# Optimization experiments

Measured on AMD Instinct MI355X. Metric: run time of the kernel, lower is better.

Reference implementation:

```python
import jax, jax.numpy as jnp
import numpy as np

B, S, H, E, TOPK = 8, 512, 1024, 8, 2


def setup_inputs() -> dict:
    key = jax.random.key(0)
    ks = jax.random.split(key, 10)
    D = 2 * H
    inp = {
        "vector": jax.random.normal(ks[0], (B, S, D), dtype=jnp.float32),
        # gate weights (Linear(H, E)): stored as [H, E] for x @ W + b
        "Wg": jax.random.normal(ks[1], (H, E), dtype=jnp.float32) * 0.02,
        "bg": jnp.zeros((E,), dtype=jnp.float32),
        "Wf": jax.random.normal(ks[2], (H, E), dtype=jnp.float32) * 0.02,
        "bf": jnp.zeros((E,), dtype=jnp.float32),
        # expert MLP weights, stacked over experts: Linear(2H,2H) -> ReLU -> Linear(2H,2H)
        "W1": jax.random.normal(ks[3], (E, D, D), dtype=jnp.float32) * 0.02,
        "b1": jnp.zeros((E, D), dtype=jnp.float32),
        "W2": jax.random.normal(ks[4], (E, D, D), dtype=jnp.float32) * 0.02,
        "b2": jnp.zeros((E, D), dtype=jnp.float32),
        # combine weights (config['initializer_weight'])
        "weight": jnp.ones((2,), dtype=jnp.float32),
        "top_k": TOPK,
    }
    return inp


def reference(vector, Wg, bg, Wf, bf, W1, b1, W2, b2, weight, top_k):
    h = Wg.shape[0]
    n_exp = Wg.shape[1]
    # gate_g on first half, softmax, then top-k sparsify (scatter of topk values)
    rout_g = jax.nn.softmax(vector[:, :, :h] @ Wg + bg, axis=-1)           # [B,S,E]
    vals, idx = jax.lax.top_k(rout_g, top_k)                               # [B,S,k]
    route_g = jnp.sum(jax.nn.one_hot(idx, n_exp, dtype=vals.dtype) * vals[..., None], axis=-2)  # [B,S,E]
    # gate_f on second half: dense softmax routing
    rout_f = jax.nn.softmax(vector[:, :, h:2 * h] @ Wf + bf, axis=-1)      # [B,S,E]
    # dense expert computation for every token (dropout = identity at eval)
    hidden = jax.nn.relu(jnp.einsum('bsd,edh->bseh', vector, W1) + b1)     # [B,S,E,2H]
    expert_out = jnp.einsum('bseh,ehd->bsed', hidden, W2) + b2             # [B,S,E,2H]
    out0 = weight[0] * jnp.einsum('bsed,bse->bsd', expert_out[..., :h], route_g)
    out1 = weight[1] * jnp.einsum('bsed,bse->bsd', expert_out[..., h:2 * h], rout_f)
    return (out0, out1)
```

## Files before the change

kernel.cpp:

```cpp
#include <hip/hip_runtime.h>

#define TOKENS 4096
#define DDIM   2048
#define HDIM   1024
#define NEXP   8
#define GK     2048
#define GN     2048

typedef __bf16 bf16_t;
typedef __bf16 bf16x8 __attribute__((ext_vector_type(8)));
typedef __bf16 bf16x4 __attribute__((ext_vector_type(4)));
typedef float  f32x4  __attribute__((ext_vector_type(4)));

__device__ inline void gld_lds16(const bf16_t* g, bf16_t* l) {
  __builtin_amdgcn_global_load_lds(
      (const __attribute__((address_space(1))) void*)g,
      (__attribute__((address_space(3))) void*)l, 16, 0, 0);
}

#define VMC(n)  asm volatile("s_waitcnt vmcnt(" #n ")" ::: "memory")
#define BAR()   __builtin_amdgcn_s_barrier()

__global__ __launch_bounds__(256)
void k_routing(const float* __restrict__ vec,
               const float* __restrict__ Wg, const float* __restrict__ bg,
               const float* __restrict__ Wf, const float* __restrict__ bfv,
               const float* __restrict__ wgt,
               float* __restrict__ c0, float* __restrict__ c1)
{
  const int wave = threadIdx.x >> 6;
  const int lane = threadIdx.x & 63;
  const int m = blockIdx.x * 4 + wave;
  const float* v = vec + (size_t)m * DDIM;

  float ag[NEXP], af[NEXP];
#pragma unroll
  for (int e = 0; e < NEXP; ++e) { ag[e] = 0.f; af[e] = 0.f; }

  for (int i = lane; i < HDIM; i += 64) {
    const float xg = v[i];
    const float xf = v[HDIM + i];
    const float4 wg0 = *(const float4*)(Wg + i * NEXP);
    const float4 wg1 = *(const float4*)(Wg + i * NEXP + 4);
    const float4 wf0 = *(const float4*)(Wf + i * NEXP);
    const float4 wf1 = *(const float4*)(Wf + i * NEXP + 4);
    ag[0] += xg * wg0.x; ag[1] += xg * wg0.y; ag[2] += xg * wg0.z; ag[3] += xg * wg0.w;
    ag[4] += xg * wg1.x; ag[5] += xg * wg1.y; ag[6] += xg * wg1.z; ag[7] += xg * wg1.w;
    af[0] += xf * wf0.x; af[1] += xf * wf0.y; af[2] += xf * wf0.z; af[3] += xf * wf0.w;
    af[4] += xf * wf1.x; af[5] += xf * wf1.y; af[6] += xf * wf1.z; af[7] += xf * wf1.w;
  }
#pragma unroll
  for (int e = 0; e < NEXP; ++e) {
#pragma unroll
    for (int off = 32; off >= 1; off >>= 1) {
      ag[e] += __shfl_xor(ag[e], off, 64);
      af[e] += __shfl_xor(af[e], off, 64);
    }
  }
  if (lane == 0) {
    float g[NEXP], f[NEXP];
    float mg = -1e30f, mf = -1e30f;
#pragma unroll
    for (int e = 0; e < NEXP; ++e) {
      g[e] = ag[e] + bg[e]; mg = fmaxf(mg, g[e]);
      f[e] = af[e] + bfv[e]; mf = fmaxf(mf, f[e]);
    }
    float sg = 0.f, sf = 0.f;
#pragma unroll
    for (int e = 0; e < NEXP; ++e) {
      g[e] = expf(g[e] - mg); sg += g[e];
      f[e] = expf(f[e] - mf); sf += f[e];
    }
    const float rg = 1.f / sg, rf = 1.f / sf;
#pragma unroll
    for (int e = 0; e < NEXP; ++e) { g[e] *= rg; f[e] *= rf; }
    int i1 = 0;
#pragma unroll
    for (int e = 1; e < NEXP; ++e) if (g[e] > g[i1]) i1 = e;
    int i2 = (i1 == 0) ? 1 : 0;
#pragma unroll
    for (int e = 0; e < NEXP; ++e) if (e != i1 && g[e] > g[i2]) i2 = e;
    const float w0 = wgt[0], w1 = wgt[1];
#pragma unroll
    for (int e = 0; e < NEXP; ++e) {
      c0[e * TOKENS + m] = (e == i1 || e == i2) ? w0 * g[e] : 0.f;
      c1[e * TOKENS + m] = w1 * f[e];
    }
  }
}

__global__ __launch_bounds__(256)
void k_cvt(const float* __restrict__ in, bf16_t* __restrict__ out)
{
  const size_t i = ((size_t)blockIdx.x * 256 + threadIdx.x) * 8;
  const float4 a = *(const float4*)(in + i);
  const float4 b = *(const float4*)(in + i + 4);
  bf16x8 o;
  o[0] = (bf16_t)a.x; o[1] = (bf16_t)a.y; o[2] = (bf16_t)a.z; o[3] = (bf16_t)a.w;
  o[4] = (bf16_t)b.x; o[5] = (bf16_t)b.y; o[6] = (bf16_t)b.z; o[7] = (bf16_t)b.w;
  *(bf16x8*)(out + i) = o;
}

#define TP 68
__global__ __launch_bounds__(256)
void k_cvt_wt(const float* __restrict__ W, bf16_t* __restrict__ Wt)
{
  __shared__ __attribute__((aligned(16))) bf16_t tile[64 * TP];
  const size_t eoff = (size_t)blockIdx.z * DDIM * DDIM;
  const float* w = W + eoff;
  bf16_t* wt = Wt + eoff;
  const int k0 = blockIdx.x * 64;
  const int n0 = blockIdx.y * 64;
  const int t = threadIdx.x;
  const int c4 = (t & 15) * 4;
  const int rb = (t >> 4) * 4;
#pragma unroll
  for (int rr = 0; rr < 4; ++rr) {
    const int r = rb + rr;
    const float4 v = *(const float4*)(w + (size_t)(k0 + r) * DDIM + n0 + c4);
    tile[(c4 + 0) * TP + r] = (bf16_t)v.x;
    tile[(c4 + 1) * TP + r] = (bf16_t)v.y;
    tile[(c4 + 2) * TP + r] = (bf16_t)v.z;
    tile[(c4 + 3) * TP + r] = (bf16_t)v.w;
  }
  __syncthreads();
  const int nl = t >> 2;
  const int kq = (t & 3) * 16;
  bf16_t* dst = wt + (size_t)(n0 + nl) * DDIM + k0 + kq;
#pragma unroll
  for (int j2 = 0; j2 < 4; ++j2) {
    bf16x4 u = *(const bf16x4*)(&tile[nl * TP + kq + j2 * 4]);
    *(bf16x4*)(dst + j2 * 4) = u;
  }
}


#define FRG(base, R, KQ) \
  (*(const bf16x8*)((base) + ((((R) * 32 + (KQ)) ^ ((((R) >> 3) & 1) << 4)))))

#define MFMA_(d, x, y) (d) = __builtin_amdgcn_mfma_f32_16x16x32_bf16((x), (y), (d), 0, 0, 0)

__global__ __launch_bounds__(512, 2)
void k_gemm1_8p(const bf16_t* __restrict__ A, const bf16_t* __restrict__ W1t,
                const float* __restrict__ b1, bf16_t* __restrict__ Hd)
{
  __shared__ __attribute__((aligned(16))) bf16_t AsF[4 * 8192];
  __shared__ __attribute__((aligned(16))) bf16_t BsF[4 * 8192];
  const int e = blockIdx.z;
  const int t = threadIdx.x;
  const int wave = t >> 6, lane = t & 63;
  const int m0 = blockIdx.x * 256, n0 = blockIdx.y * 256;
  const int wm = (wave >> 2) * 128, wn = (wave & 3) * 64;
  const int fr = lane & 15, kq = (lane >> 4) * 8;

  const int sRw = wave * 16 + (lane >> 2);
  const int sC  = ((lane & 3) * 8) ^ (((lane >> 5) & 1) << 4);
  const bf16_t* aSrc = A + (size_t)(m0 + sRw) * GK + sC;
  const bf16_t* bSrc = W1t + (size_t)e * GN * GK + (size_t)(n0 + sRw) * GK + sC;
  bf16_t* aDst = AsF + wave * 512;
  bf16_t* bDst = BsF + wave * 512;

#define STA1(P, U) do { const bf16_t* _s = aSrc + (size_t)(P) * 32; \
    gld_lds16(_s, aDst + (U) * 8192); \
    gld_lds16(_s + (size_t)128 * GK, aDst + (U) * 8192 + 4096); } while (0)
#define STB1(P, U) do { const bf16_t* _s = bSrc + (size_t)(P) * 32; \
    gld_lds16(_s, bDst + (U) * 8192); \
    gld_lds16(_s + (size_t)128 * GK, bDst + (U) * 8192 + 4096); } while (0)

  f32x4 acc[8][4] = {};

#define PH1(U, SP, SU, DOST) do { \
    bf16x8 a_[8], b_[4]; \
    _Pragma("unroll") \
    for (int _j = 0; _j < 4; ++_j) b_[_j] = FRG(BsF + (U) * 8192, wn + _j * 16 + fr, kq); \
    _Pragma("unroll") \
    for (int _i = 0; _i < 8; ++_i) a_[_i] = FRG(AsF + (U) * 8192, wm + _i * 16 + fr, kq); \
    if (DOST) { STA1(SP, SU); STB1(SP, SU); } \
    __builtin_amdgcn_s_setprio(1); \
    _Pragma("unroll") \
    for (int _i = 0; _i < 8; ++_i) \
      _Pragma("unroll") \
      for (int _j = 0; _j < 4; ++_j) MFMA_(acc[_i][_j], a_[_i], b_[_j]); \
    __builtin_amdgcn_s_setprio(0); \
  } while (0)

  STA1(0, 0); STB1(0, 0);
  STA1(1, 1); STB1(1, 1);
  STA1(2, 2); STB1(2, 2);
  VMC(8); BAR();

#pragma unroll 1
  for (int pb = 0; pb < 60; pb += 4) {
    PH1(0, pb + 3, 3, 1); VMC(8); BAR();
    PH1(1, pb + 4, 0, 1); VMC(8); BAR();
    PH1(2, pb + 5, 1, 1); VMC(8); BAR();
    PH1(3, pb + 6, 2, 1); VMC(8); BAR();
  }
  PH1(0, 63, 3, 1); VMC(8); BAR();
  PH1(1, 0, 0, 0);  VMC(4); BAR();
  PH1(2, 0, 0, 0);  VMC(0); BAR();
  PH1(3, 0, 0, 0);

  const float* bias = b1 + (size_t)e * DDIM;
  bf16_t* Hb = Hd + (size_t)e * TOKENS * DDIM;
  const int ecol = lane & 15, erow = (lane >> 4) * 4;
#pragma unroll
  for (int j = 0; j < 4; ++j) {
    const int gn = n0 + wn + j * 16 + ecol;
    const float bv = bias[gn];
#pragma unroll
    for (int i = 0; i < 8; ++i) {
      const int gm = m0 + wm + i * 16 + erow;
#pragma unroll
      for (int r = 0; r < 4; ++r) {
        float v = acc[i][j][r] + bv;
        v = v > 0.f ? v : 0.f;
        Hb[(size_t)(gm + r) * DDIM + gn] = (bf16_t)v;
      }
    }
  }
#undef PH1
#undef STA1
#undef STB1
}

__global__ __launch_bounds__(512, 2)
void k_gemm2_8p(const bf16_t* __restrict__ Hd, const bf16_t* __restrict__ W2t,
                const float* __restrict__ b2,
                const float* __restrict__ c0, const float* __restrict__ c1,
                float* __restrict__ out0, float* __restrict__ out1)
{
  __shared__ __attribute__((aligned(16))) bf16_t AsF[4 * 4096];
  __shared__ __attribute__((aligned(16))) bf16_t BsF[4 * 8192];
  __shared__ float cs[NEXP][128];
  __shared__ float bsh[NEXP][256];

  const int t = threadIdx.x;
  const int wave = t >> 6, lane = t & 63;
  const int m0 = blockIdx.x * 128, n0 = blockIdx.y * 256;
  const int wm = (wave >> 2) * 64, wn = (wave & 3) * 64;
  const int fr = lane & 15, kq = (lane >> 4) * 8;
  const bool hi = (n0 >= HDIM);
  const float* cc = hi ? c1 : c0;

  for (int idx = t; idx < NEXP * 128; idx += 512) {
    const int ee = idx >> 7, r = idx & 127;
    cs[ee][r] = cc[ee * TOKENS + m0 + r];
  }
  for (int idx = t; idx < NEXP * 256; idx += 512) {
    const int ee = idx >> 8, r = idx & 255;
    bsh[ee][r] = b2[ee * DDIM + n0 + r];
  }
  __syncthreads();

  const int sRw = wave * 16 + (lane >> 2);
  const int sC  = ((lane & 3) * 8) ^ (((lane >> 5) & 1) << 4);
  const bf16_t* aSrc = Hd + (size_t)(m0 + sRw) * GK + sC;
  const bf16_t* bSrc = W2t + (size_t)(n0 + sRw) * GK + sC;
  bf16_t* aDst = AsF + wave * 512;
  bf16_t* bDst = BsF + wave * 512;

#define STA2(P, U) do { \
    const bf16_t* _s = aSrc + (size_t)((P) >> 6) * ((size_t)TOKENS * GK) + (size_t)((P) & 63) * 32; \
    gld_lds16(_s, aDst + (U) * 4096); } while (0)
#define STB2(P, U) do { \
    const bf16_t* _s = bSrc + (size_t)((P) >> 6) * ((size_t)GN * GK) + (size_t)((P) & 63) * 32; \
    gld_lds16(_s, bDst + (U) * 8192); \
    gld_lds16(_s + (size_t)128 * GK, bDst + (U) * 8192 + 4096); } while (0)

  f32x4 acc[4][4] = {};
  f32x4 fin[4][4] = {};

#define PH2(U, SP, SU, DOST) do { \
    bf16x8 a_[4], b_[4]; \
    _Pragma("unroll") \
    for (int _j = 0; _j < 4; ++_j) b_[_j] = FRG(BsF + (U) * 8192, wn + _j * 16 + fr, kq); \
    _Pragma("unroll") \
    for (int _i = 0; _i < 4; ++_i) a_[_i] = FRG(AsF + (U) * 4096, wm + _i * 16 + fr, kq); \
    if (DOST) { STA2(SP, SU); STB2(SP, SU); } \
    __builtin_amdgcn_s_setprio(1); \
    _Pragma("unroll") \
    for (int _i = 0; _i < 4; ++_i) \
      _Pragma("unroll") \
      for (int _j = 0; _j < 4; ++_j) MFMA_(acc[_i][_j], a_[_i], b_[_j]); \
    __builtin_amdgcn_s_setprio(0); \
  } while (0)

  const int ecol = lane & 15, erow = (lane >> 4) * 4;

#define FOLD2(E) do { \
    _Pragma("unroll") \
    for (int _j = 0; _j < 4; ++_j) { \
      const float _bv = bsh[E][wn + _j * 16 + ecol]; \
      _Pragma("unroll") \
      for (int _i = 0; _i < 4; ++_i) { \
        const int _rw = wm + _i * 16 + erow; \
        _Pragma("unroll") \
        for (int _r = 0; _r < 4; ++_r) { \
          fin[_i][_j][_r] += cs[E][_rw + _r] * (acc[_i][_j][_r] + _bv); \
          acc[_i][_j][_r] = 0.f; \
        } \
      } \
    } \
  } while (0)

  STA2(0, 0); STB2(0, 0);
  STA2(1, 1); STB2(1, 1);
  STA2(2, 2); STB2(2, 2);
  VMC(6); BAR();

#pragma unroll 1
  for (int pb = 0; pb < 508; pb += 4) {
    PH2(0, pb + 3, 3, 1); VMC(6); BAR();
    PH2(1, pb + 4, 0, 1); VMC(6); BAR();
    PH2(2, pb + 5, 1, 1); VMC(6); BAR();
    PH2(3, pb + 6, 2, 1);
    if ((pb & 63) == 60) FOLD2((pb + 3) >> 6);
    VMC(6); BAR();
  }
  PH2(0, 511, 3, 1); VMC(6); BAR();
  PH2(1, 0, 0, 0);  VMC(3); BAR();
  PH2(2, 0, 0, 0);  VMC(0); BAR();
  PH2(3, 0, 0, 0);
  FOLD2(7);

#pragma unroll
  for (int j = 0; j < 4; ++j) {
    const int gn = n0 + wn + j * 16 + ecol;
    float* ob = hi ? (out1 + (gn - HDIM)) : (out0 + gn);
#pragma unroll
    for (int i = 0; i < 4; ++i) {
      const int gm = m0 + wm + i * 16 + erow;
#pragma unroll
      for (int r = 0; r < 4; ++r)
        ob[(size_t)(gm + r) * HDIM] = fin[i][j][r];
    }
  }
#undef PH2
#undef STA2
#undef STB2
#undef FOLD2
}

__global__ __launch_bounds__(256, 2)
void k_gemm_relu(const bf16_t* __restrict__ A, const bf16_t* __restrict__ W1t,
                 const float* __restrict__ b1, bf16_t* __restrict__ Hd)
{
  __shared__ __attribute__((aligned(16))) bf16_t As[128 * 32];
  __shared__ __attribute__((aligned(16))) bf16_t Bs[128 * 32];
  const int e = blockIdx.z;
  const bf16_t* Bt = W1t + (size_t)e * GK * GN;
  const float* bias = b1 + (size_t)e * GN;
  bf16_t* H = Hd + (size_t)e * TOKENS * GN;

  const int t = threadIdx.x;
  const int wave = t >> 6;
  const int lane = t & 63;
  const int m0 = blockIdx.x * 128;
  const int n0 = blockIdx.y * 128;
  const int wm = (wave >> 1) << 6;
  const int wn = (wave & 1) << 6;

  f32x4 acc[4][4] = {};

  const bf16_t* aP0 = A + (size_t)(m0 + (t >> 2)) * GK + (t & 3) * 8;
  const bf16_t* aP1 = aP0 + (size_t)64 * GK;
  const bf16_t* bP0 = Bt + (size_t)(n0 + (t >> 2)) * GK + (t & 3) * 8;
  const bf16_t* bP1 = bP0 + (size_t)64 * GK;
  bf16_t* lA0 = As + wave * 512;
  bf16_t* lA1 = As + 2048 + wave * 512;
  bf16_t* lB0 = Bs + wave * 512;
  bf16_t* lB1 = Bs + 2048 + wave * 512;

  const int fr = lane & 15;
  const int kq = (lane >> 4) * 8;

  for (int k0 = 0; k0 < GK; k0 += 32) {
    gld_lds16(aP0 + k0, lA0);
    gld_lds16(aP1 + k0, lA1);
    gld_lds16(bP0 + k0, lB0);
    gld_lds16(bP1 + k0, lB1);
    __syncthreads();
    bf16x8 afr[4], bfr[4];
#pragma unroll
    for (int i = 0; i < 4; ++i) {
      afr[i] = *(const bf16x8*)(As + (wm + i * 16 + fr) * 32 + kq);
      bfr[i] = *(const bf16x8*)(Bs + (wn + i * 16 + fr) * 32 + kq);
    }
#pragma unroll
    for (int i = 0; i < 4; ++i)
#pragma unroll
      for (int j = 0; j < 4; ++j)
        acc[i][j] = __builtin_amdgcn_mfma_f32_16x16x32_bf16(afr[i], bfr[j], acc[i][j], 0, 0, 0);
    __syncthreads();
  }

  const int col = lane & 15;
  const int rq  = (lane >> 4) * 4;
#pragma unroll
  for (int j = 0; j < 4; ++j) {
    const int gn = n0 + wn + j * 16 + col;
    const float bv = bias[gn];
#pragma unroll
    for (int i = 0; i < 4; ++i) {
      const int gm = m0 + wm + i * 16 + rq;
#pragma unroll
      for (int r = 0; r < 4; ++r) {
        float v = acc[i][j][r] + bv;
        v = v > 0.f ? v : 0.f;
        H[(size_t)(gm + r) * GN + gn] = (bf16_t)v;
      }
    }
  }
}

__global__ __launch_bounds__(256, 2)
void k_gemm_out(const bf16_t* __restrict__ A, const bf16_t* __restrict__ Bt,
                const float* __restrict__ bias,
                const float* __restrict__ c0, const float* __restrict__ c1,
                float* __restrict__ out0, float* __restrict__ out1, const int accum)
{
  __shared__ __attribute__((aligned(16))) bf16_t As[128 * 32];
  __shared__ __attribute__((aligned(16))) bf16_t Bs[128 * 32];
  const int t = threadIdx.x;
  const int wave = t >> 6;
  const int lane = t & 63;
  const int m0 = blockIdx.x * 128;
  const int n0 = blockIdx.y * 128;
  const int wm = (wave >> 1) << 6;
  const int wn = (wave & 1) << 6;

  f32x4 acc[4][4] = {};

  const bf16_t* aP0 = A + (size_t)(m0 + (t >> 2)) * GK + (t & 3) * 8;
  const bf16_t* aP1 = aP0 + (size_t)64 * GK;
  const bf16_t* bP0 = Bt + (size_t)(n0 + (t >> 2)) * GK + (t & 3) * 8;
  const bf16_t* bP1 = bP0 + (size_t)64 * GK;
  bf16_t* lA0 = As + wave * 512;
  bf16_t* lA1 = As + 2048 + wave * 512;
  bf16_t* lB0 = Bs + wave * 512;
  bf16_t* lB1 = Bs + 2048 + wave * 512;

  const int fr = lane & 15;
  const int kq = (lane >> 4) * 8;

  for (int k0 = 0; k0 < GK; k0 += 32) {
    gld_lds16(aP0 + k0, lA0);
    gld_lds16(aP1 + k0, lA1);
    gld_lds16(bP0 + k0, lB0);
    gld_lds16(bP1 + k0, lB1);
    __syncthreads();
    bf16x8 afr[4], bfr[4];
#pragma unroll
    for (int i = 0; i < 4; ++i) {
      afr[i] = *(const bf16x8*)(As + (wm + i * 16 + fr) * 32 + kq);
      bfr[i] = *(const bf16x8*)(Bs + (wn + i * 16 + fr) * 32 + kq);
    }
#pragma unroll
    for (int i = 0; i < 4; ++i)
#pragma unroll
      for (int j = 0; j < 4; ++j)
        acc[i][j] = __builtin_amdgcn_mfma_f32_16x16x32_bf16(afr[i], bfr[j], acc[i][j], 0, 0, 0);
    __syncthreads();
  }

  const int col = lane & 15;
  const int rq  = (lane >> 4) * 4;
#pragma unroll
  for (int j = 0; j < 4; ++j) {
    const int gn = n0 + wn + j * 16 + col;
    const float bv = bias[gn];
    const bool lo = gn < HDIM;
    float* obase = lo ? (out0 + gn) : (out1 + (gn - HDIM));
    const float* cc = lo ? c0 : c1;
#pragma unroll
    for (int i = 0; i < 4; ++i) {
      const int gmB = m0 + wm + i * 16 + rq;
#pragma unroll
      for (int r = 0; r < 4; ++r) {
        const int gm = gmB + r;
        float v = (acc[i][j][r] + bv) * cc[gm];
        float* dst = obase + (size_t)gm * HDIM;
        if (accum) v += *dst;
        *dst = v;
      }
    }
  }
}

extern "C" void kernel_launch(void* const* d_in, const int* in_sizes, int n_in,
                              void* d_out, int out_size, void* d_ws, size_t ws_size,
                              hipStream_t stream)
{
  const float* vec = (const float*)d_in[0];
  const float* Wg  = (const float*)d_in[1];
  const float* bg  = (const float*)d_in[2];
  const float* Wf  = (const float*)d_in[3];
  const float* bfv = (const float*)d_in[4];
  const float* W1  = (const float*)d_in[5];
  const float* b1  = (const float*)d_in[6];
  const float* W2  = (const float*)d_in[7];
  const float* b2  = (const float*)d_in[8];
  const float* wgt = (const float*)d_in[9];

  float* out0 = (float*)d_out;
  float* out1 = out0 + (size_t)TOKENS * HDIM;

  char* base = (char*)d_ws;
  const size_t XB = (size_t)TOKENS * DDIM * 2;
  const size_t HB = (size_t)NEXP * TOKENS * DDIM * 2;
  const size_t WT = (size_t)NEXP * DDIM * DDIM * 2;

  bf16_t* Xbf = (bf16_t*)base;
  float*  c0  = (float*)(base + XB);
  float*  c1  = c0 + (size_t)NEXP * TOKENS;
  size_t off = XB + 2 * (size_t)NEXP * TOKENS * 4;

  k_routing<<<dim3(TOKENS / 4), 256, 0, stream>>>(vec, Wg, bg, Wf, bfv, wgt, c0, c1);
  k_cvt<<<dim3((TOKENS * DDIM) / 2048), 256, 0, stream>>>(vec, Xbf);

  if (ws_size >= off + HB + 2 * WT) {
    bf16_t* hidden = (bf16_t*)(base + off);
    bf16_t* W1t    = (bf16_t*)(base + off + HB);
    bf16_t* W2t    = (bf16_t*)(base + off + HB + WT);
    k_cvt_wt<<<dim3(32, 32, NEXP), 256, 0, stream>>>(W1, W1t);
    k_cvt_wt<<<dim3(32, 32, NEXP), 256, 0, stream>>>(W2, W2t);
    k_gemm1_8p<<<dim3(16, 8, NEXP), 512, 0, stream>>>(Xbf, W1t, b1, hidden);
    k_gemm2_8p<<<dim3(32, 8), 512, 0, stream>>>(hidden, W2t, b2, c0, c1, out0, out1);
  } else {
    bf16_t* hidden = (bf16_t*)(base + off);
    bf16_t* W1t    = hidden + (size_t)TOKENS * DDIM;
    bf16_t* W2t    = W1t + (size_t)DDIM * DDIM;
    for (int e = 0; e < NEXP; ++e) {
      k_cvt_wt<<<dim3(32, 32, 1), 256, 0, stream>>>(W1 + (size_t)e * DDIM * DDIM, W1t);
      k_cvt_wt<<<dim3(32, 32, 1), 256, 0, stream>>>(W2 + (size_t)e * DDIM * DDIM, W2t);
      k_gemm_relu<<<dim3(32, 16, 1), 256, 0, stream>>>(Xbf, W1t, b1 + (size_t)e * DDIM, hidden);
      k_gemm_out<<<dim3(32, 16), 256, 0, stream>>>(
          hidden, W2t, b2 + (size_t)e * DDIM,
          c0 + (size_t)e * TOKENS, c1 + (size_t)e * TOKENS, out0, out1, e > 0);
    }
  }
}
```

Before: 951.0 us.

## Double-buffer LDS fragment registers to overlap reads with MFMA in both GEMMs

Both expert GEMM kernels now keep two register sets of A/B fragments and read the next LDS stage into one set while MFMAs consume the other. Each global-to-LDS stage load is issued before those reads, and the vmcnt waits are tightened to match. The aim is to hide LDS read latency behind matrix instructions instead of stalling on it before every MFMA block. The cost is roughly double the fragment registers (notably 24 bf16x8 in gemm1), which may pressure occupancy or cause spills. The stage-to-buffer ordering also becomes more delicate, so any off-by-one in the waits would race.

```diff
diff --git a/kernel.cpp b/kernel.cpp
--- a/kernel.cpp
+++ b/kernel.cpp
@@ -160,46 +160,51 @@
   bf16_t* aDst = AsF + wave * 512;
   bf16_t* bDst = BsF + wave * 512;
 
-#define STA1(P, U) do { const bf16_t* _s = aSrc + (size_t)(P) * 32; \
-    gld_lds16(_s, aDst + (U) * 8192); \
-    gld_lds16(_s + (size_t)128 * GK, aDst + (U) * 8192 + 4096); } while (0)
-#define STB1(P, U) do { const bf16_t* _s = bSrc + (size_t)(P) * 32; \
-    gld_lds16(_s, bDst + (U) * 8192); \
-    gld_lds16(_s + (size_t)128 * GK, bDst + (U) * 8192 + 4096); } while (0)
+#define STG1(P, U) do { const bf16_t* _sa = aSrc + (size_t)(P) * 32; \
+    const bf16_t* _sb = bSrc + (size_t)(P) * 32; \
+    gld_lds16(_sa, aDst + (U) * 8192); \
+    gld_lds16(_sa + (size_t)128 * GK, aDst + (U) * 8192 + 4096); \
+    gld_lds16(_sb, bDst + (U) * 8192); \
+    gld_lds16(_sb + (size_t)128 * GK, bDst + (U) * 8192 + 4096); } while (0)
 
   f32x4 acc[8][4] = {};
-
-#define PH1(U, SP, SU, DOST) do { \
-    bf16x8 a_[8], b_[4]; \
-    _Pragma("unroll") \
-    for (int _j = 0; _j < 4; ++_j) b_[_j] = FRG(BsF + (U) * 8192, wn + _j * 16 + fr, kq); \
-    _Pragma("unroll") \
-    for (int _i = 0; _i < 8; ++_i) a_[_i] = FRG(AsF + (U) * 8192, wm + _i * 16 + fr, kq); \
-    if (DOST) { STA1(SP, SU); STB1(SP, SU); } \
+  bf16x8 fAa[8], fAb[4], fBa[8], fBb[4];
+
+#define RD1(SET, U) do { \
+    _Pragma("unroll") \
+    for (int _j = 0; _j < 4; ++_j) SET##b[_j] = FRG(BsF + (U) * 8192, wn + _j * 16 + fr, kq); \
+    _Pragma("unroll") \
+    for (int _i = 0; _i < 8; ++_i) SET##a[_i] = FRG(AsF + (U) * 8192, wm + _i * 16 + fr, kq); \
+  } while (0)
+
+#define MM1(SET) do { \
     __builtin_amdgcn_s_setprio(1); \
     _Pragma("unroll") \
     for (int _i = 0; _i < 8; ++_i) \
       _Pragma("unroll") \
-      for (int _j = 0; _j < 4; ++_j) MFMA_(acc[_i][_j], a_[_i], b_[_j]); \
+      for (int _j = 0; _j < 4; ++_j) MFMA_(acc[_i][_j], SET##a[_i], SET##b[_j]); \
     __builtin_amdgcn_s_setprio(0); \
   } while (0)
 
-  STA1(0, 0); STB1(0, 0);
-  STA1(1, 1); STB1(1, 1);
-  STA1(2, 2); STB1(2, 2);
-  VMC(8); BAR();
+  STG1(0, 0); STG1(1, 1); STG1(2, 2);
+  VMC(4); BAR();
+  RD1(fA, 0);
 
 #pragma unroll 1
-  for (int pb = 0; pb < 60; pb += 4) {
-    PH1(0, pb + 3, 3, 1); VMC(8); BAR();
-    PH1(1, pb + 4, 0, 1); VMC(8); BAR();
-    PH1(2, pb + 5, 1, 1); VMC(8); BAR();
-    PH1(3, pb + 6, 2, 1); VMC(8); BAR();
-  }
-  PH1(0, 63, 3, 1); VMC(8); BAR();
-  PH1(1, 0, 0, 0);  VMC(4); BAR();
-  PH1(2, 0, 0, 0);  VMC(0); BAR();
-  PH1(3, 0, 0, 0);
+  for (int pb = 0; pb < 56; pb += 4) {
+    STG1(pb + 3, 3); RD1(fB, 1); MM1(fA); VMC(4); BAR();
+    STG1(pb + 4, 0); RD1(fA, 2); MM1(fB); VMC(4); BAR();
+    STG1(pb + 5, 1); RD1(fB, 3); MM1(fA); VMC(4); BAR();
+    STG1(pb + 6, 2); RD1(fA, 0); MM1(fB); VMC(4); BAR();
+  }
+  STG1(59, 3); RD1(fB, 1); MM1(fA); VMC(4); BAR();
+  STG1(60, 0); RD1(fA, 2); MM1(fB); VMC(4); BAR();
+  STG1(61, 1); RD1(fB, 3); MM1(fA); VMC(4); BAR();
+  STG1(62, 2); RD1(fA, 0); MM1(fB); VMC(4); BAR();
+  STG1(63, 3); RD1(fB, 1); MM1(fA); VMC(4); BAR();
+  RD1(fA, 2); MM1(fB); VMC(0); BAR();
+  RD1(fB, 3); MM1(fA); BAR();
+  MM1(fB);
 
   const float* bias = b1 + (size_t)e * DDIM;
   bf16_t* Hb = Hd + (size_t)e * TOKENS * DDIM;
@@ -219,9 +224,9 @@
       }
     }
   }
-#undef PH1
-#undef STA1
-#undef STB1
+#undef RD1
+#undef MM1
+#undef STG1
 }
 
 __global__ __launch_bounds__(512, 2)
@@ -260,29 +265,30 @@
   bf16_t* aDst = AsF + wave * 512;
   bf16_t* bDst = BsF + wave * 512;
 
-#define STA2(P, U) do { \
-    const bf16_t* _s = aSrc + (size_t)((P) >> 6) * ((size_t)TOKENS * GK) + (size_t)((P) & 63) * 32; \
-    gld_lds16(_s, aDst + (U) * 4096); } while (0)
-#define STB2(P, U) do { \
-    const bf16_t* _s = bSrc + (size_t)((P) >> 6) * ((size_t)GN * GK) + (size_t)((P) & 63) * 32; \
-    gld_lds16(_s, bDst + (U) * 8192); \
-    gld_lds16(_s + (size_t)128 * GK, bDst + (U) * 8192 + 4096); } while (0)
+#define STG2(P, U) do { \
+    const bf16_t* _sa = aSrc + (size_t)((P) >> 6) * ((size_t)TOKENS * GK) + (size_t)((P) & 63) * 32; \
+    const bf16_t* _sb = bSrc + (size_t)((P) >> 6) * ((size_t)GN * GK) + (size_t)((P) & 63) * 32; \
+    gld_lds16(_sa, aDst + (U) * 4096); \
+    gld_lds16(_sb, bDst + (U) * 8192); \
+    gld_lds16(_sb + (size_t)128 * GK, bDst + (U) * 8192 + 4096); } while (0)
 
   f32x4 acc[4][4] = {};
   f32x4 fin[4][4] = {};
-
-#define PH2(U, SP, SU, DOST) do { \
-    bf16x8 a_[4], b_[4]; \
-    _Pragma("unroll") \
-    for (int _j = 0; _j < 4; ++_j) b_[_j] = FRG(BsF + (U) * 8192, wn + _j * 16 + fr, kq); \
-    _Pragma("unroll") \
-    for (int _i = 0; _i < 4; ++_i) a_[_i] = FRG(AsF + (U) * 4096, wm + _i * 16 + fr, kq); \
-    if (DOST) { STA2(SP, SU); STB2(SP, SU); } \
+  bf16x8 fAa[4], fAb[4], fBa[4], fBb[4];
+
+#define RD2(SET, U) do { \
+    _Pragma("unroll") \
+    for (int _j = 0; _j < 4; ++_j) SET##b[_j] = FRG(BsF + (U) * 8192, wn + _j * 16 + fr, kq); \
+    _Pragma("unroll") \
+    for (int _i = 0; _i < 4; ++_i) SET##a[_i] = FRG(AsF + (U) * 4096, wm + _i * 16 + fr, kq); \
+  } while (0)
+
+#define MM2(SET) do { \
     __builtin_amdgcn_s_setprio(1); \
     _Pragma("unroll") \
     for (int _i = 0; _i < 4; ++_i) \
       _Pragma("unroll") \
-      for (int _j = 0; _j < 4; ++_j) MFMA_(acc[_i][_j], a_[_i], b_[_j]); \
+      for (int _j = 0; _j < 4; ++_j) MFMA_(acc[_i][_j], SET##a[_i], SET##b[_j]); \
     __builtin_amdgcn_s_setprio(0); \
   } while (0)
 
@@ -304,24 +310,27 @@
     } \
   } while (0)
 
-  STA2(0, 0); STB2(0, 0);
-  STA2(1, 1); STB2(1, 1);
-  STA2(2, 2); STB2(2, 2);
-  VMC(6); BAR();
+  STG2(0, 0); STG2(1, 1); STG2(2, 2);
+  VMC(3); BAR();
+  RD2(fA, 0);
 
 #pragma unroll 1
-  for (int pb = 0; pb < 508; pb += 4) {
-    PH2(0, pb + 3, 3, 1); VMC(6); BAR();
-    PH2(1, pb + 4, 0, 1); VMC(6); BAR();
-    PH2(2, pb + 5, 1, 1); VMC(6); BAR();
-    PH2(3, pb + 6, 2, 1);
-    if ((pb & 63) == 60) FOLD2((pb + 3) >> 6);
-    VMC(6); BAR();
-  }
-  PH2(0, 511, 3, 1); VMC(6); BAR();
-  PH2(1, 0, 0, 0);  VMC(3); BAR();
-  PH2(2, 0, 0, 0);  VMC(0); BAR();
-  PH2(3, 0, 0, 0);
+  for (int pb = 0; pb < 504; pb += 4) {
+    STG2(pb + 3, 3); RD2(fB, 1); MM2(fA); VMC(3); BAR();
+    STG2(pb + 4, 0); RD2(fA, 2); MM2(fB); VMC(3); BAR();
+    STG2(pb + 5, 1); RD2(fB, 3); MM2(fA); VMC(3); BAR();
+    STG2(pb + 6, 2); RD2(fA, 0); MM2(fB);
+    if (((pb + 3) & 63) == 63) FOLD2((pb + 3) >> 6);
+    VMC(3); BAR();
+  }
+  STG2(507, 3); RD2(fB, 1); MM2(fA); VMC(3); BAR();
+  STG2(508, 0); RD2(fA, 2); MM2(fB); VMC(3); BAR();
+  STG2(509, 1); RD2(fB, 3); MM2(fA); VMC(3); BAR();
+  STG2(510, 2); RD2(fA, 0); MM2(fB); VMC(3); BAR();
+  STG2(511, 3); RD2(fB, 1); MM2(fA); VMC(3); BAR();
+  RD2(fA, 2); MM2(fB); VMC(0); BAR();
+  RD2(fB, 3); MM2(fA); BAR();
+  MM2(fB);
   FOLD2(7);
 
 #pragma unroll
@@ -336,9 +345,9 @@
         ob[(size_t)(gm + r) * HDIM] = fin[i][j][r];
     }
   }
-#undef PH2
-#undef STA2
-#undef STB2
+#undef RD2
+#undef MM2
+#undef STG2
 #undef FOLD2
 }
 
```

Result: slower. 1.064 ms (+11.8%).
